# Kernel optimization log

Hardware: AMD Instinct MI355X
Metric: run time of the kernel (lower is better)

## Reference

```python
import jax, jax.numpy as jnp
import numpy as np

B, T, D = 4, 2048, 1024
H, DH = 16, 64

def setup_inputs() -> dict:
    key = jax.random.key(0)
    k1, k2, k3 = jax.random.split(key, 3)
    x = jax.random.normal(k1, (B, T, D), dtype=jnp.float32)
    ln_gamma = jnp.ones((D,), dtype=jnp.float32)
    ln_beta = jnp.zeros((D,), dtype=jnp.float32)
    W_qkv = jax.random.normal(k2, (3 * D, D), dtype=jnp.float32) * (1.0 / np.sqrt(D))
    W_o = jax.random.normal(k3, (D, D), dtype=jnp.float32) * (1.0 / np.sqrt(D))
    return {"x": x, "ln_gamma": ln_gamma, "ln_beta": ln_beta, "W_qkv": W_qkv, "W_o": W_o}

def reference(x, ln_gamma, ln_beta, W_qkv, W_o):
    b, t, d = x.shape
    scale = 1.0 / np.sqrt(DH)
    # pre-LN in fp32 (eps=1e-5, elementwise affine)
    xf = x.astype(jnp.float32)
    mu = jnp.mean(xf, axis=-1, keepdims=True)
    var = jnp.mean(jnp.square(xf - mu), axis=-1, keepdims=True)
    xn = (xf - mu) * jax.lax.rsqrt(var + 1e-5) * ln_gamma + ln_beta
    xn = xn.astype(x.dtype)
    # fused QKV projection (torch Linear: y = x @ W^T), view as (B,T,H,3*DH)
    qkv = jnp.einsum('btd,ed->bte', xn, W_qkv).reshape(b, t, H, 3 * DH)
    Q, K, V = jnp.split(qkv, 3, axis=-1)  # each (B,T,H,DH)
    # scores (B,H,T,T), causal mask, softmax
    scores = jnp.einsum('bqhd,bkhd->bhqk', Q, K) * scale
    causal = jnp.tril(jnp.ones((t, t), dtype=bool))
    scores = jnp.where(causal, scores, -jnp.inf)
    A = jax.nn.softmax(scores, axis=-1)
    ctx = jnp.einsum('bhqk,bkhd->bqhd', A, V).reshape(b, t, d)
    return jnp.einsum('btd,ed->bte', ctx, W_o)
```

## Files before the change

### kernel.cpp

```cpp
#include <hip/hip_runtime.h>


typedef __attribute__((ext_vector_type(8))) short bf8v;
typedef __attribute__((ext_vector_type(4))) float f4v;

#define Tt  2048
#define Dd  1024
#define Hh  16
#define DHh 64

#if __has_builtin(__builtin_amdgcn_exp2f)
#define EXP2(x) __builtin_amdgcn_exp2f(x)
#else
#define EXP2(x) __expf((x) * 0.69314718056f)
#endif

__device__ __forceinline__ ushort f2bf(float f) {
  union { float f; unsigned v; } c; c.f = f;
  unsigned r = c.v + 0x7fffu + ((c.v >> 16) & 1u);
  return (ushort)(r >> 16);
}
__device__ __forceinline__ ushort f2bf_rn(float f) {
  union { float f; unsigned v; } c; c.f = f;
  return (ushort)((c.v + 0x8000u) >> 16);
}
__device__ __forceinline__ f4v zero4() { f4v z; z[0]=z[1]=z[2]=z[3]=0.f; return z; }

__device__ __forceinline__ void gl_lds16(const ushort* g, ushort* l) {
  __builtin_amdgcn_global_load_lds(
      (const __attribute__((address_space(1))) unsigned*)g,
      (__attribute__((address_space(3))) unsigned*)l, 16, 0, 0);
}

__global__ __launch_bounds__(256)
void cvt_k(const float* __restrict__ src, ushort* __restrict__ dst) {
  const int i = blockIdx.x * 256 + threadIdx.x;
  const float4 v = ((const float4*)src)[i];
  ushort4 o;
  o.x = f2bf(v.x); o.y = f2bf(v.y); o.z = f2bf(v.z); o.w = f2bf(v.w);
  ((ushort4*)dst)[i] = o;
}

__global__ __launch_bounds__(256)
void ln_k(const float* __restrict__ x, const float* __restrict__ g,
          const float* __restrict__ bta, ushort* __restrict__ xn) {
  const int row = blockIdx.x, tid = threadIdx.x;
  const float4 v = ((const float4*)(x + row * Dd))[tid];
  float s  = v.x + v.y + v.z + v.w;
  float sq = v.x*v.x + v.y*v.y + v.z*v.z + v.w*v.w;
  #pragma unroll
  for (int off = 32; off; off >>= 1) {
    s  += __shfl_down(s,  off, 64);
    sq += __shfl_down(sq, off, 64);
  }
  __shared__ float red[8];
  const int w = tid >> 6, l = tid & 63;
  if (l == 0) { red[w] = s; red[w + 4] = sq; }
  __syncthreads();
  s  = red[0] + red[1] + red[2] + red[3];
  sq = red[4] + red[5] + red[6] + red[7];
  const float mu  = s * (1.0f / Dd);
  const float var = sq * (1.0f / Dd) - mu * mu;
  const float rs  = rsqrtf(var + 1e-5f);
  const float4 gv = ((const float4*)g)[tid];
  const float4 bv = ((const float4*)bta)[tid];
  ushort4 o;
  o.x = f2bf((v.x - mu) * rs * gv.x + bv.x);
  o.y = f2bf((v.y - mu) * rs * gv.y + bv.y);
  o.z = f2bf((v.z - mu) * rs * gv.z + bv.z);
  o.w = f2bf((v.w - mu) * rs * gv.w + bv.w);
  ((ushort4*)(xn + row * Dd))[tid] = o;
}

template<int MODE>
__global__ __launch_bounds__(256)
void gemm128(const ushort* __restrict__ A, const ushort* __restrict__ Bt,
             void* __restrict__ O0v, ushort* __restrict__ O1, ushort* __restrict__ O2,
             int Kd, int nbm) {
  __shared__ ushort As[2][128 * 64], Bs[2][128 * 64];
  const int tid = threadIdx.x;
  const int l = tid & 63, w = tid >> 6, fr = l & 15, fq = l >> 4;
  const int wm = w & 1, wn = w >> 1;
  const int bm = blockIdx.x % nbm, bn = blockIdx.x / nbm;
  const int gr8 = l >> 3, gc8s = ((l & 7) ^ gr8) * 8;
  const int sw = fr & 7;
  const int cA = (fq ^ sw) * 8, cB = ((4 + fq) ^ sw) * 8;
  const int NIT = Kd >> 6;

  f4v acc[4][4];
  #pragma unroll
  for (int m = 0; m < 4; m++)
    #pragma unroll
    for (int n = 0; n < 4; n++) acc[m][n] = zero4();

  auto stage = [&](int it, int bi) {
    const int k0 = it * 64;
    #pragma unroll
    for (int i = 0; i < 4; i++) {
      const int row = w * 32 + i * 8;
      gl_lds16(A  + (bm * 128 + row + gr8) * Kd + k0 + gc8s, &As[bi][row * 64]);
      gl_lds16(Bt + (bn * 128 + row + gr8) * Kd + k0 + gc8s, &Bs[bi][row * 64]);
    }
  };

  stage(0, 0);
  for (int it = 0; it < NIT; ++it) {
    __syncthreads();
    if (it + 1 < NIT) stage(it + 1, (it + 1) & 1);
    const ushort* Ab = As[it & 1];
    const ushort* Bb = Bs[it & 1];
    #pragma unroll
    for (int kk = 0; kk < 2; kk++) {
      const int cs = kk ? cB : cA;
      bf8v af[4], bf[4];
      #pragma unroll
      for (int m = 0; m < 4; m++)
        af[m] = *(const bf8v*)&Ab[(wm * 64 + m * 16 + fr) * 64 + cs];
      #pragma unroll
      for (int n = 0; n < 4; n++)
        bf[n] = *(const bf8v*)&Bb[(wn * 64 + n * 16 + fr) * 64 + cs];
      #pragma unroll
      for (int m = 0; m < 4; m++)
        #pragma unroll
        for (int n = 0; n < 4; n++)
          acc[m][n] = __builtin_amdgcn_mfma_f32_16x16x32_bf16(af[m], bf[n], acc[m][n], 0, 0, 0);
    }
  }

  #pragma unroll
  for (int m = 0; m < 4; m++) {
    const int grow = bm * 128 + wm * 64 + m * 16 + fq * 4;
    #pragma unroll
    for (int n = 0; n < 4; n++) {
      const int e = bn * 128 + wn * 64 + n * 16 + fr;
      #pragma unroll
      for (int r = 0; r < 4; r++) {
        const int row = grow + r;
        if (MODE == 0) {
          const int h = e / 192, inner = e % 192;
          const int sel = inner >> 6, dh = inner & 63;
          const int bb = row >> 11, t = row & 2047;
          float v = acc[m][n][r];
          if (sel == 0) v *= 0.18033688f;
          ushort* dst = (sel == 0) ? (ushort*)O0v : (sel == 1) ? O1 : O2;
          dst[((bb * Hh + h) * Tt + t) * DHh + dh] = f2bf(v);
        } else {
          ((float*)O0v)[row * Dd + e] = acc[m][n][r];
        }
      }
    }
  }
}

__global__ __launch_bounds__(256)
void vtr_k(const ushort* __restrict__ Vb, ushort* __restrict__ Vtg) {
  __shared__ ushort tile[64 * 72];
  const int tid = threadIdx.x;
  const int tt = blockIdx.x & 31;
  const int hb = blockIdx.x >> 5;
  const int base = hb * Tt * DHh;
  const int srow = tid >> 3, soff = (tid & 7) * 8;
  #pragma unroll
  for (int i = 0; i < 2; i++) {
    const int t = srow + i * 32;
    const uint4 vv = *(const uint4*)(Vb + base + (tt * 64 + t) * DHh + soff);
    const ushort* e = (const ushort*)&vv;
    #pragma unroll
    for (int j = 0; j < 8; j++) tile[(soff + j) * 72 + t] = e[j];
  }
  __syncthreads();
  #pragma unroll
  for (int i = 0; i < 2; i++) {
    const int dh = srow + i * 32;
    *(uint4*)(Vtg + base + dh * Tt + tt * 64 + soff) = *(const uint4*)&tile[dh * 72 + soff];
  }
}

__global__ __launch_bounds__(512)
void attn_k(const ushort* __restrict__ Qb, const ushort* __restrict__ Kb,
            const ushort* __restrict__ Vtg, ushort* __restrict__ ctx) {
  __shared__ ushort QP[128 * 68];
  __shared__ ushort Ks[2][64 * 64], Vt[2][64 * 64];
  const int tid = threadIdx.x;
  const int l = tid & 63, w = tid >> 6, fr = l & 15, fq = l >> 4;
  const int bid = blockIdx.x;
  const int hb = (bid & 7) * 8 + (bid >> 6);
  const int u  = (bid >> 3) & 7;
  const int h  = hb & 15, b = hb >> 4;
  const int headbase = hb * Tt * DHh;
  const int gr8 = l >> 3, gc8s = ((l & 7) ^ gr8) * 8;
  const int sw = fr & 7;
  const int cA = (fq ^ sw) * 8, cB = ((4 + fq) ^ sw) * 8;

  auto stageKV = [&](int kt, int bi) {
    const int row = w * 8;
    gl_lds16(Kb  + headbase + (kt * 64 + row + gr8) * DHh + gc8s, &Ks[bi][row * 64]);
    gl_lds16(Vtg + headbase + (row + gr8) * Tt + kt * 64 + gc8s, &Vt[bi][row * 64]);
  };

  for (int half = 0; half < 2; ++half) {
    const int qt = half ? (15 - u) : u;
    const int qrow0w = qt * 128 + w * 16;

    if (half) __syncthreads();

    #pragma unroll
    for (int i = 0; i < 2; i++) {
      const int row = w * 16 + i * 8;
      gl_lds16(Qb + headbase + (qt * 128 + row + gr8) * DHh + gc8s, &QP[row * 64]);
    }
    stageKV(0, 0);
    __syncthreads();

    bf8v aq[2];
    aq[0] = *(const bf8v*)&QP[(w * 16 + fr) * 64 + cA];
    aq[1] = *(const bf8v*)&QP[(w * 16 + fr) * 64 + cB];
    __asm__ __volatile__("" ::: "memory");

    f4v o[4];
    #pragma unroll
    for (int n = 0; n < 4; n++) o[n] = zero4();
    float lsum = 0.f;

    const int ktmax = 2 * qt + 1;
    for (int kt = 0; kt <= ktmax; ++kt) {
      if (kt) __syncthreads();
      if (kt < ktmax) stageKV(kt + 1, (kt + 1) & 1);
      const ushort* K_ = Ks[kt & 1];
      const ushort* V_ = Vt[kt & 1];

      if (kt * 64 <= qrow0w + 15) {
        f4v scT[4];
        #pragma unroll
        for (int n = 0; n < 4; n++) scT[n] = zero4();
        __builtin_amdgcn_s_setprio(1);
        #pragma unroll
        for (int nt = 0; nt < 4; nt++) {
          const bf8v k0 = *(const bf8v*)&K_[(nt * 16 + fr) * 64 + cA];
          const bf8v k1 = *(const bf8v*)&K_[(nt * 16 + fr) * 64 + cB];
          scT[nt] = __builtin_amdgcn_mfma_f32_16x16x32_bf16(k0, aq[0], scT[nt], 0, 0, 0);
          scT[nt] = __builtin_amdgcn_mfma_f32_16x16x32_bf16(k1, aq[1], scT[nt], 0, 0, 0);
        }
        __builtin_amdgcn_s_setprio(0);

        if (kt * 64 + 63 > qrow0w) {
          const int q0 = qrow0w + fr;
          #pragma unroll
          for (int nt = 0; nt < 4; nt++) {
            const int kc0 = kt * 64 + nt * 16 + fq * 4;
            #pragma unroll
            for (int r = 0; r < 4; r++)
              if (kc0 + r > q0) scT[nt][r] = -1e30f;
          }
        }

        {
          const int prow = w * 16 + fr;
          ushort* pbase = &QP[prow * 68 + fq * 4];
          #pragma unroll
          for (int nt = 0; nt < 4; nt++) {
            const float p0 = EXP2(scT[nt][0]), p1 = EXP2(scT[nt][1]);
            const float p2 = EXP2(scT[nt][2]), p3 = EXP2(scT[nt][3]);
            ushort4 pk;
            pk.x = f2bf_rn(p0); pk.y = f2bf_rn(p1);
            pk.z = f2bf_rn(p2); pk.w = f2bf_rn(p3);
            *(ushort4*)(pbase + nt * 16) = pk;
            lsum += (p0 + p1) + (p2 + p3);
          }
        }

        __asm__ __volatile__("" ::: "memory");

        __builtin_amdgcn_s_setprio(1);
        #pragma unroll
        for (int s = 0; s < 2; s++) {
          const bf8v ap = *(const bf8v*)&QP[(w * 16 + fr) * 68 + s * 32 + fq * 8];
          #pragma unroll
          for (int nt = 0; nt < 4; nt++) {
            const bf8v bv2 = *(const bf8v*)&V_[(nt * 16 + fr) * 64 + (s ? cB : cA)];
            o[nt] = __builtin_amdgcn_mfma_f32_16x16x32_bf16(ap, bv2, o[nt], 0, 0, 0);
          }
        }
        __builtin_amdgcn_s_setprio(0);
      }
    }

    float t = lsum;
    t += __shfl_xor(t, 16, 64);
    t += __shfl_xor(t, 32, 64);
    const float inv = 1.0f / t;
    #pragma unroll
    for (int r = 0; r < 4; r++) {
      const float iv = __shfl(inv, 20 * fq + r, 64);
      const int rowg = b * Tt + qt * 128 + w * 16 + fq * 4 + r;
      #pragma unroll
      for (int nt = 0; nt < 4; nt++)
        ctx[rowg * Dd + h * DHh + nt * 16 + fr] = f2bf(o[nt][r] * iv);
    }
  }
}

extern "C" void kernel_launch(void* const* d_in, const int* in_sizes, int n_in,
                              void* d_out, int out_size, void* d_ws, size_t ws_size,
                              hipStream_t stream) {
  const float* x    = (const float*)d_in[0];
  const float* g    = (const float*)d_in[1];
  const float* bta  = (const float*)d_in[2];
  const float* wqkv = (const float*)d_in[3];
  const float* wo   = (const float*)d_in[4];

  const int NROW = 4 * Tt;
  const int NQ   = 4 * Hh * Tt * DHh;
  ushort* xn   = (ushort*)d_ws;
  ushort* Qb   = xn + NROW * Dd;
  ushort* Kb   = Qb + NQ;
  ushort* Vb   = Kb + NQ;
  ushort* ctx  = Vb + NQ;
  ushort* wqkb = ctx + NROW * Dd;
  ushort* wob  = wqkb + 3 * Dd * Dd;
  ushort* VbT  = xn;

  cvt_k<<<3 * Dd * Dd / 1024, 256, 0, stream>>>(wqkv, wqkb);
  cvt_k<<<Dd * Dd / 1024, 256, 0, stream>>>(wo, wob);
  ln_k<<<NROW, 256, 0, stream>>>(x, g, bta, xn);
  gemm128<0><<<64 * 24, 256, 0, stream>>>(xn, wqkb, Qb, Kb, Vb, Dd, 64);
  vtr_k<<<4 * Hh * (Tt / 64), 256, 0, stream>>>(Vb, VbT);
  attn_k<<<4 * Hh * (Tt / 128) / 2, 512, 0, stream>>>(Qb, Kb, VbT, ctx);
  gemm128<1><<<64 * 8, 256, 0, stream>>>(ctx, wob, (void*)d_out, nullptr, nullptr, Dd, 64);
}
```

Baseline: 238.6 us.

## Use 128x256 GEMM tiles with 8 waves and triple-buffered vmcnt pipeline

Widens both projection GEMMs to 128x256 output tiles with 512 threads, so each block reuses its A tile across twice as many columns. The K loop becomes a 3-stage global-to-LDS pipeline that waits on vmcnt counts at a raw barrier instead of a full __syncthreads per step, keeping two stages in flight. The attention kernel gets separate Q and P shared buffers instead of one aliased buffer. In exchange, LDS use rises to about 144KB per GEMM block, limiting occupancy to one block per CU, and the grids shrink to 768 and 256 blocks, which may leave wave-quantization gaps.

```diff
diff --git a/kernel.cpp b/kernel.cpp
--- a/kernel.cpp
+++ b/kernel.cpp
@@ -31,6 +31,14 @@
       (const __attribute__((address_space(1))) unsigned*)g,
       (__attribute__((address_space(3))) unsigned*)l, 16, 0, 0);
 }
+
+#define PIPE_BARRIER(cnt_asm)                                   \
+  do {                                                          \
+    asm volatile(cnt_asm ::: "memory");                         \
+    __builtin_amdgcn_sched_barrier(0);                          \
+    __builtin_amdgcn_s_barrier();                               \
+    __builtin_amdgcn_sched_barrier(0);                          \
+  } while (0)
 
 __global__ __launch_bounds__(256)
 void cvt_k(const float* __restrict__ src, ushort* __restrict__ dst) {
@@ -73,11 +81,12 @@
 }
 
 template<int MODE>
-__global__ __launch_bounds__(256)
-void gemm128(const ushort* __restrict__ A, const ushort* __restrict__ Bt,
+__global__ __launch_bounds__(512)
+void gemm256(const ushort* __restrict__ A, const ushort* __restrict__ Bt,
              void* __restrict__ O0v, ushort* __restrict__ O1, ushort* __restrict__ O2,
              int Kd, int nbm) {
-  __shared__ ushort As[2][128 * 64], Bs[2][128 * 64];
+  __shared__ ushort As[3][128 * 64];
+  __shared__ ushort Bs[3][256 * 64];
   const int tid = threadIdx.x;
   const int l = tid & 63, w = tid >> 6, fr = l & 15, fq = l >> 4;
   const int wm = w & 1, wn = w >> 1;
@@ -96,19 +105,26 @@
   auto stage = [&](int it, int bi) {
     const int k0 = it * 64;
     #pragma unroll
+    for (int i = 0; i < 2; i++) {
+      const int row = w * 16 + i * 8;
+      gl_lds16(A + (bm * 128 + row + gr8) * Kd + k0 + gc8s, &As[bi][row * 64]);
+    }
+    #pragma unroll
     for (int i = 0; i < 4; i++) {
       const int row = w * 32 + i * 8;
-      gl_lds16(A  + (bm * 128 + row + gr8) * Kd + k0 + gc8s, &As[bi][row * 64]);
-      gl_lds16(Bt + (bn * 128 + row + gr8) * Kd + k0 + gc8s, &Bs[bi][row * 64]);
+      gl_lds16(Bt + (bn * 256 + row + gr8) * Kd + k0 + gc8s, &Bs[bi][row * 64]);
     }
   };
 
   stage(0, 0);
+  stage(1, 1);
+  int cb = 0;
   for (int it = 0; it < NIT; ++it) {
-    __syncthreads();
-    if (it + 1 < NIT) stage(it + 1, (it + 1) & 1);
-    const ushort* Ab = As[it & 1];
-    const ushort* Bb = Bs[it & 1];
+    if (it + 1 < NIT) PIPE_BARRIER("s_waitcnt vmcnt(6) lgkmcnt(0)");
+    else              PIPE_BARRIER("s_waitcnt vmcnt(0) lgkmcnt(0)");
+    if (it + 2 < NIT) { int sb = cb + 2; if (sb >= 3) sb -= 3; stage(it + 2, sb); }
+    const ushort* Ab = As[cb];
+    const ushort* Bb = Bs[cb];
     #pragma unroll
     for (int kk = 0; kk < 2; kk++) {
       const int cs = kk ? cB : cA;
@@ -125,6 +141,7 @@
         for (int n = 0; n < 4; n++)
           acc[m][n] = __builtin_amdgcn_mfma_f32_16x16x32_bf16(af[m], bf[n], acc[m][n], 0, 0, 0);
     }
+    if (++cb == 3) cb = 0;
   }
 
   #pragma unroll
@@ -132,7 +149,7 @@
     const int grow = bm * 128 + wm * 64 + m * 16 + fq * 4;
     #pragma unroll
     for (int n = 0; n < 4; n++) {
-      const int e = bn * 128 + wn * 64 + n * 16 + fr;
+      const int e = bn * 256 + wn * 64 + n * 16 + fr;
       #pragma unroll
       for (int r = 0; r < 4; r++) {
         const int row = grow + r;
@@ -179,7 +196,8 @@
 __global__ __launch_bounds__(512)
 void attn_k(const ushort* __restrict__ Qb, const ushort* __restrict__ Kb,
             const ushort* __restrict__ Vtg, ushort* __restrict__ ctx) {
-  __shared__ ushort QP[128 * 68];
+  __shared__ ushort QS[128 * 64];
+  __shared__ ushort Pb[128 * 68];
   __shared__ ushort Ks[2][64 * 64], Vt[2][64 * 64];
   const int tid = threadIdx.x;
   const int l = tid & 63, w = tid >> 6, fr = l & 15, fq = l >> 4;
@@ -207,14 +225,14 @@
     #pragma unroll
     for (int i = 0; i < 2; i++) {
       const int row = w * 16 + i * 8;
-      gl_lds16(Qb + headbase + (qt * 128 + row + gr8) * DHh + gc8s, &QP[row * 64]);
+      gl_lds16(Qb + headbase + (qt * 128 + row + gr8) * DHh + gc8s, &QS[row * 64]);
     }
     stageKV(0, 0);
     __syncthreads();
 
     bf8v aq[2];
-    aq[0] = *(const bf8v*)&QP[(w * 16 + fr) * 64 + cA];
-    aq[1] = *(const bf8v*)&QP[(w * 16 + fr) * 64 + cB];
+    aq[0] = *(const bf8v*)&QS[(w * 16 + fr) * 64 + cA];
+    aq[1] = *(const bf8v*)&QS[(w * 16 + fr) * 64 + cB];
     __asm__ __volatile__("" ::: "memory");
 
     f4v o[4];
@@ -256,7 +274,7 @@
 
         {
           const int prow = w * 16 + fr;
-          ushort* pbase = &QP[prow * 68 + fq * 4];
+          ushort* pbase = &Pb[prow * 68 + fq * 4];
           #pragma unroll
           for (int nt = 0; nt < 4; nt++) {
             const float p0 = EXP2(scT[nt][0]), p1 = EXP2(scT[nt][1]);
@@ -274,7 +292,7 @@
         __builtin_amdgcn_s_setprio(1);
         #pragma unroll
         for (int s = 0; s < 2; s++) {
-          const bf8v ap = *(const bf8v*)&QP[(w * 16 + fr) * 68 + s * 32 + fq * 8];
+          const bf8v ap = *(const bf8v*)&Pb[(w * 16 + fr) * 68 + s * 32 + fq * 8];
           #pragma unroll
           for (int nt = 0; nt < 4; nt++) {
             const bf8v bv2 = *(const bf8v*)&V_[(nt * 16 + fr) * 64 + (s ? cB : cA)];
@@ -323,8 +341,8 @@
   cvt_k<<<3 * Dd * Dd / 1024, 256, 0, stream>>>(wqkv, wqkb);
   cvt_k<<<Dd * Dd / 1024, 256, 0, stream>>>(wo, wob);
   ln_k<<<NROW, 256, 0, stream>>>(x, g, bta, xn);
-  gemm128<0><<<64 * 24, 256, 0, stream>>>(xn, wqkb, Qb, Kb, Vb, Dd, 64);
+  gemm256<0><<<64 * 12, 512, 0, stream>>>(xn, wqkb, Qb, Kb, Vb, Dd, 64);
   vtr_k<<<4 * Hh * (Tt / 64), 256, 0, stream>>>(Vb, VbT);
   attn_k<<<4 * Hh * (Tt / 128) / 2, 512, 0, stream>>>(Qb, Kb, VbT, ctx);
-  gemm128<1><<<64 * 8, 256, 0, stream>>>(ctx, wob, (void*)d_out, nullptr, nullptr, Dd, 64);
-}
+  gemm256<1><<<64 * 4, 512, 0, stream>>>(ctx, wob, (void*)d_out, nullptr, nullptr, Dd, 64);
+}
```

After: 258.7 us. +8.4%, slower.
